# Performance work log

Measured on AMD Instinct MI355X. Metric: run time of the kernel, lower is better.

The kernel has to match this reference:

```python
import jax, jax.numpy as jnp
import numpy as np

DISTANCE_W = 1.0
ANGLE_W = 1.0
EPS = 1e-12  # matches F.normalize eps


def setup_inputs() -> dict:
    key = jax.random.key(0)
    k1, k2 = jax.random.split(key)
    student_emb = jax.random.normal(k1, (1024, 512), dtype=jnp.float32)
    teacher_emb = jax.random.normal(k2, (1024, 512), dtype=jnp.float32)
    return {"student_emb": student_emb, "teacher_emb": teacher_emb}


def _pairwise_similarity(emb):
    # F.normalize(emb, dim=1) then emb @ emb.T -> [N, N] cosine similarity
    norm = jnp.maximum(jnp.linalg.norm(emb, axis=1, keepdims=True), EPS)
    en = emb / norm
    return en @ en.T


def _angle_similarity(emb):
    # ||e_i - e_j||^2 for all pairs, computed via the GEMM expansion
    # (same math as the N x N x D broadcast in the original, no O(N^2 D) tensor)
    sq = jnp.sum(emb * emb, axis=1)  # [N]
    gram = emb @ emb.T               # [N, N]
    return sq[:, None] + sq[None, :] - 2.0 * gram


def reference(student_emb, teacher_emb):
    loss_dist = jnp.mean((_pairwise_similarity(student_emb) - _pairwise_similarity(teacher_emb)) ** 2)
    loss_angle = jnp.mean((_angle_similarity(student_emb) - _angle_similarity(teacher_emb)) ** 2)
    return DISTANCE_W * loss_dist + ANGLE_W * loss_angle
```

## Files before the change

kernel.cpp:

```cpp
#include <hip/hip_runtime.h>

typedef short short8 __attribute__((ext_vector_type(8)));
typedef float f32x16 __attribute__((ext_vector_type(16)));
typedef unsigned short ushort;
typedef unsigned long long u64;

#define DD 512
#define NBLK 272
#define MAGIC 0x9E3779B97F4A7C15ULL


__device__ __forceinline__ short to_bf16(float f) {
    unsigned int u = __float_as_uint(f);
    u += 0x7FFFu + ((u >> 16) & 1u);
    return (short)(u >> 16);
}

__device__ __forceinline__ short8 pack8(float4 a, float4 b) {
    short8 r;
    r[0] = to_bf16(a.x); r[1] = to_bf16(a.y); r[2] = to_bf16(a.z); r[3] = to_bf16(a.w);
    r[4] = to_bf16(b.x); r[5] = to_bf16(b.y); r[6] = to_bf16(b.z); r[7] = to_bf16(b.w);
    return r;
}

__device__ __forceinline__ float dot4(float4 v) {
    return v.x*v.x + v.y*v.y + v.z*v.z + v.w*v.w;
}

__global__ __launch_bounds__(128) void rkd_one(const float* __restrict__ S,
                                               const float* __restrict__ T,
                                               u64* __restrict__ done_tag,
                                               float* __restrict__ done_val,
                                               float* __restrict__ out) {
    __shared__ ushort tiles[2][12288];
    __shared__ float statI[4][32];
    __shared__ float statJ[4][64];
    __shared__ float wsum[2];

    const int t   = threadIdx.x;
    const int blk = blockIdx.x;

    int rem = blk, a = 0;
    for (;;) { int cnt = 16 - (a >> 1); if (rem < cnt) break; rem -= cnt; ++a; }
    const int b2 = (a >> 1) + rem;
    const int I = a * 32;
    const int J = b2 * 64;

    const int w = t >> 6;
    const int L = t & 63;
    const int c = L & 31;
    const int h = L >> 5;
    const int colsel = w * 32;
    const int lrow   = L >> 3;
    const int c8     = (L & 7) ^ lrow;

    const float* gsrc[12];
    int ldst[12];
    #pragma unroll
    for (int j = 0; j < 12; ++j) {
        const int q = w * 12 + j;
        const float* gm; int gbase, lo, sub;
        if (q < 4)       { gm = S; gbase = I; sub = q;      lo = 0;    }
        else if (q < 8)  { gm = T; gbase = I; sub = q - 4;  lo = 2048; }
        else if (q < 16) { gm = S; gbase = J; sub = q - 8;  lo = 4096; }
        else             { gm = T; gbase = J; sub = q - 16; lo = 8192; }
        gsrc[j] = gm + (size_t)(gbase + sub * 8 + lrow) * DD + c8 * 8;
        ldst[j] = lo + sub * 512 + L * 8;
    }

    float4 rv[12][2];
    float  sqp[12];
    #pragma unroll
    for (int j = 0; j < 12; ++j) sqp[j] = 0.0f;

    f32x16 accS, accT;
    #pragma unroll
    for (int i2 = 0; i2 < 16; ++i2) { accS[i2] = 0.0f; accT[i2] = 0.0f; }

    #pragma unroll
    for (int j = 0; j < 12; ++j) {
        rv[j][0] = ((const float4*)gsrc[j])[0];
        rv[j][1] = ((const float4*)gsrc[j])[1];
    }

    for (int i = 0; i < 8; ++i) {
        __syncthreads();
        ushort* db = &tiles[i & 1][0];
        #pragma unroll
        for (int j = 0; j < 12; ++j) {
            sqp[j] += dot4(rv[j][0]) + dot4(rv[j][1]);
            *(short8*)(db + ldst[j]) = pack8(rv[j][0], rv[j][1]);
        }
        __syncthreads();
        if (i < 7) {
            #pragma unroll
            for (int j = 0; j < 12; ++j) {
                rv[j][0] = ((const float4*)(gsrc[j] + (i + 1) * 64))[0];
                rv[j][1] = ((const float4*)(gsrc[j] + (i + 1) * 64))[1];
            }
        }
        const ushort* base = &tiles[i & 1][0];
        #pragma unroll
        for (int step = 0; step < 4; ++step) {
            const int us = ((step * 2 + h) ^ (c & 7)) * 8;
            short8 afS = *(const short8*)(base + c * 64 + us);
            short8 afT = *(const short8*)(base + 2048 + c * 64 + us);
            short8 bS8 = *(const short8*)(base + 4096 + (colsel + c) * 64 + us);
            short8 bT8 = *(const short8*)(base + 8192 + (colsel + c) * 64 + us);
            accS = __builtin_amdgcn_mfma_f32_32x32x16_bf16(afS, bS8, accS, 0, 0, 0);
            accT = __builtin_amdgcn_mfma_f32_32x32x16_bf16(afT, bT8, accT, 0, 0, 0);
        }
    }

    #pragma unroll
    for (int j = 0; j < 12; ++j) {
        float s = sqp[j];
        s += __shfl_xor(s, 1);
        s += __shfl_xor(s, 2);
        s += __shfl_xor(s, 4);
        if ((L & 7) == 0) {
            const float rn = 1.0f / fmaxf(sqrtf(s), 1e-12f);
            const int q = w * 12 + j;
            if (q < 4)       { statI[0][q*8        + lrow] = s; statI[2][q*8        + lrow] = rn; }
            else if (q < 8)  { statI[1][(q-4)*8    + lrow] = s; statI[3][(q-4)*8    + lrow] = rn; }
            else if (q < 16) { statJ[0][(q-8)*8    + lrow] = s; statJ[2][(q-8)*8    + lrow] = rn; }
            else             { statJ[1][(q-16)*8   + lrow] = s; statJ[3][(q-16)*8   + lrow] = rn; }
        }
    }
    __syncthreads();

    const int colg = colsel + c;
    const int jg   = J + colg;
    const float js  = statJ[0][colg], jt  = statJ[1][colg];
    const float rjs = statJ[2][colg], rjt = statJ[3][colg];

    float local = 0.0f;
    #pragma unroll
    for (int reg = 0; reg < 16; ++reg) {
        const int rowg = (reg & 3) + 8 * (reg >> 2) + 4 * h;
        const int ig = I + rowg;
        float wgt = (jg > ig) ? 2.0f : ((jg == ig) ? 1.0f : 0.0f);
        float is  = statI[0][rowg], it  = statI[1][rowg];
        float ris = statI[2][rowg], rit = statI[3][rowg];
        float gs = accS[reg], gt = accT[reg];
        float d1 = gs * ris * rjs - gt * rit * rjt;
        float d2 = (is + js - 2.0f * gs) - (it + jt - 2.0f * gt);
        local += wgt * (d1 * d1 + d2 * d2);
    }

    #pragma unroll
    for (int off = 32; off > 0; off >>= 1) local += __shfl_down(local, off);
    if (L == 0) wsum[w] = local;
    __syncthreads();

    if (t == 0) {
        done_val[blk] = wsum[0] + wsum[1];
        __threadfence();
        __hip_atomic_store(&done_tag[blk], MAGIC,
                           __ATOMIC_RELAXED, __HIP_MEMORY_SCOPE_AGENT);
    }

    if (blk == NBLK - 1) {
        for (int i2 = t; i2 < NBLK; i2 += 128)
            while (__hip_atomic_load(&done_tag[i2], __ATOMIC_RELAXED,
                                     __HIP_MEMORY_SCOPE_AGENT) != MAGIC)
                __builtin_amdgcn_s_sleep(2);
        __syncthreads();
        __threadfence();
        float part = 0.0f;
        for (int i2 = t; i2 < NBLK; i2 += 128) part += done_val[i2];
        #pragma unroll
        for (int off = 32; off > 0; off >>= 1) part += __shfl_down(part, off);
        if ((t & 63) == 0) wsum[t >> 6] = part;
        __syncthreads();
        if (t == 0) out[0] = (wsum[0] + wsum[1]) * (1.0f / 1048576.0f);
    }
}

extern "C" void kernel_launch(void* const* d_in, const int* in_sizes, int n_in,
                              void* d_out, int out_size, void* d_ws, size_t ws_size,
                              hipStream_t stream) {
    const float* S = (const float*)d_in[0];
    const float* T = (const float*)d_in[1];
    char* ws = (char*)d_ws;
    u64*   done_tag = (u64*)ws;
    float* done_val = (float*)(ws + 4096);

    rkd_one<<<NBLK, 128, 0, stream>>>(S, T, done_tag, done_val, (float*)d_out);
}
```

Before: 83.38 us.

## Stage fp32 tiles via direct global-to-LDS loads and convert at MFMA time

Replaces the register-staged load, convert and LDS store pipeline with async global_load_lds that copies fp32 data straight into shared memory with double buffering. Conversion to bf16 moves to the MFMA operand read and uses the packed v_cvt_pk_bf16_f32 instruction. Row squared norms are now accumulated from the LDS-read fragments. This drops VGPR pressure and one barrier per iteration, at the cost of twice the LDS traffic for fp32 tiles, twice the k-iterations, and redundant conversions across waves.

```diff
diff --git a/kernel.cpp b/kernel.cpp
--- a/kernel.cpp
+++ b/kernel.cpp
@@ -3,6 +3,7 @@
 typedef short short8 __attribute__((ext_vector_type(8)));
 typedef float f32x16 __attribute__((ext_vector_type(16)));
 typedef unsigned short ushort;
+typedef unsigned int u32;
 typedef unsigned long long u64;
 
 #define DD 512
@@ -10,17 +11,19 @@
 #define MAGIC 0x9E3779B97F4A7C15ULL
 
 
-__device__ __forceinline__ short to_bf16(float f) {
-    unsigned int u = __float_as_uint(f);
-    u += 0x7FFFu + ((u >> 16) & 1u);
-    return (short)(u >> 16);
+__device__ __forceinline__ u32 cvt_pk_bf16(float lo, float hi) {
+    u32 r;
+    asm("v_cvt_pk_bf16_f32 %0, %1, %2" : "=v"(r) : "v"(lo), "v"(hi));
+    return r;
 }
 
-__device__ __forceinline__ short8 pack8(float4 a, float4 b) {
-    short8 r;
-    r[0] = to_bf16(a.x); r[1] = to_bf16(a.y); r[2] = to_bf16(a.z); r[3] = to_bf16(a.w);
-    r[4] = to_bf16(b.x); r[5] = to_bf16(b.y); r[6] = to_bf16(b.z); r[7] = to_bf16(b.w);
-    return r;
+__device__ __forceinline__ short8 pack_bf8(float4 a, float4 b) {
+    union { u32 u[4]; short8 s; } r;
+    r.u[0] = cvt_pk_bf16(a.x, a.y);
+    r.u[1] = cvt_pk_bf16(a.z, a.w);
+    r.u[2] = cvt_pk_bf16(b.x, b.y);
+    r.u[3] = cvt_pk_bf16(b.z, b.w);
+    return r.s;
 }
 
 __device__ __forceinline__ float dot4(float4 v) {
@@ -32,7 +35,7 @@
                                                u64* __restrict__ done_tag,
                                                float* __restrict__ done_val,
                                                float* __restrict__ out) {
-    __shared__ ushort tiles[2][12288];
+    __shared__ float tiles[2][6144];
     __shared__ float statI[4][32];
     __shared__ float statJ[4][64];
     __shared__ float wsum[2];
@@ -61,70 +64,73 @@
         const int q = w * 12 + j;
         const float* gm; int gbase, lo, sub;
         if (q < 4)       { gm = S; gbase = I; sub = q;      lo = 0;    }
-        else if (q < 8)  { gm = T; gbase = I; sub = q - 4;  lo = 2048; }
-        else if (q < 16) { gm = S; gbase = J; sub = q - 8;  lo = 4096; }
-        else             { gm = T; gbase = J; sub = q - 16; lo = 8192; }
-        gsrc[j] = gm + (size_t)(gbase + sub * 8 + lrow) * DD + c8 * 8;
-        ldst[j] = lo + sub * 512 + L * 8;
+        else if (q < 8)  { gm = T; gbase = I; sub = q - 4;  lo = 1024; }
+        else if (q < 16) { gm = S; gbase = J; sub = q - 8;  lo = 2048; }
+        else             { gm = T; gbase = J; sub = q - 16; lo = 4096; }
+        gsrc[j] = gm + (size_t)(gbase + sub * 8 + lrow) * DD + c8 * 4;
+        ldst[j] = lo + sub * 256 + L * 4;
     }
-
-    float4 rv[12][2];
-    float  sqp[12];
-    #pragma unroll
-    for (int j = 0; j < 12; ++j) sqp[j] = 0.0f;
 
     f32x16 accS, accT;
     #pragma unroll
     for (int i2 = 0; i2 < 16; ++i2) { accS[i2] = 0.0f; accT[i2] = 0.0f; }
+    float sqp[4] = {0.0f, 0.0f, 0.0f, 0.0f};
 
     #pragma unroll
-    for (int j = 0; j < 12; ++j) {
-        rv[j][0] = ((const float4*)gsrc[j])[0];
-        rv[j][1] = ((const float4*)gsrc[j])[1];
-    }
+    for (int j = 0; j < 12; ++j)
+        __builtin_amdgcn_global_load_lds(
+            (const __attribute__((address_space(1))) void*)(gsrc[j]),
+            (__attribute__((address_space(3))) void*)(&tiles[0][0] + ldst[j]), 16, 0, 0);
 
-    for (int i = 0; i < 8; ++i) {
+    for (int i = 0; i < 16; ++i) {
         __syncthreads();
-        ushort* db = &tiles[i & 1][0];
+        if (i < 15) {
+            const int k0 = (i + 1) * 32;
+            float* nb = &tiles[(i + 1) & 1][0];
+            #pragma unroll
+            for (int j = 0; j < 12; ++j)
+                __builtin_amdgcn_global_load_lds(
+                    (const __attribute__((address_space(1))) void*)(gsrc[j] + k0),
+                    (__attribute__((address_space(3))) void*)(nb + ldst[j]), 16, 0, 0);
+        }
+        const float* base = &tiles[i & 1][0];
+        const float* Ar = base + c * 32;
+        const float* Br = base + (colsel + c) * 32;
         #pragma unroll
-        for (int j = 0; j < 12; ++j) {
-            sqp[j] += dot4(rv[j][0]) + dot4(rv[j][1]);
-            *(short8*)(db + ldst[j]) = pack8(rv[j][0], rv[j][1]);
-        }
-        __syncthreads();
-        if (i < 7) {
-            #pragma unroll
-            for (int j = 0; j < 12; ++j) {
-                rv[j][0] = ((const float4*)(gsrc[j] + (i + 1) * 64))[0];
-                rv[j][1] = ((const float4*)(gsrc[j] + (i + 1) * 64))[1];
-            }
-        }
-        const ushort* base = &tiles[i & 1][0];
-        #pragma unroll
-        for (int step = 0; step < 4; ++step) {
-            const int us = ((step * 2 + h) ^ (c & 7)) * 8;
-            short8 afS = *(const short8*)(base + c * 64 + us);
-            short8 afT = *(const short8*)(base + 2048 + c * 64 + us);
-            short8 bS8 = *(const short8*)(base + 4096 + (colsel + c) * 64 + us);
-            short8 bT8 = *(const short8*)(base + 8192 + (colsel + c) * 64 + us);
-            accS = __builtin_amdgcn_mfma_f32_32x32x16_bf16(afS, bS8, accS, 0, 0, 0);
-            accT = __builtin_amdgcn_mfma_f32_32x32x16_bf16(afT, bT8, accT, 0, 0, 0);
+        for (int s = 0; s < 2; ++s) {
+            const int oc0 = (((s * 4) + h * 2)     ^ (c & 7)) * 4;
+            const int oc1 = (((s * 4) + h * 2 + 1) ^ (c & 7)) * 4;
+            float4 a0 = *(const float4*)(Ar + oc0);
+            float4 a1 = *(const float4*)(Ar + oc1);
+            float4 t0 = *(const float4*)(Ar + 1024 + oc0);
+            float4 t1 = *(const float4*)(Ar + 1024 + oc1);
+            float4 b0 = *(const float4*)(Br + 2048 + oc0);
+            float4 b1 = *(const float4*)(Br + 2048 + oc1);
+            float4 u0 = *(const float4*)(Br + 4096 + oc0);
+            float4 u1 = *(const float4*)(Br + 4096 + oc1);
+            sqp[0] += dot4(a0) + dot4(a1);
+            sqp[1] += dot4(t0) + dot4(t1);
+            sqp[2] += dot4(b0) + dot4(b1);
+            sqp[3] += dot4(u0) + dot4(u1);
+            accS = __builtin_amdgcn_mfma_f32_32x32x16_bf16(pack_bf8(a0, a1),
+                                                           pack_bf8(b0, b1), accS, 0, 0, 0);
+            accT = __builtin_amdgcn_mfma_f32_32x32x16_bf16(pack_bf8(t0, t1),
+                                                           pack_bf8(u0, u1), accT, 0, 0, 0);
         }
     }
 
-    #pragma unroll
-    for (int j = 0; j < 12; ++j) {
-        float s = sqp[j];
-        s += __shfl_xor(s, 1);
-        s += __shfl_xor(s, 2);
-        s += __shfl_xor(s, 4);
-        if ((L & 7) == 0) {
-            const float rn = 1.0f / fmaxf(sqrtf(s), 1e-12f);
-            const int q = w * 12 + j;
-            if (q < 4)       { statI[0][q*8        + lrow] = s; statI[2][q*8        + lrow] = rn; }
-            else if (q < 8)  { statI[1][(q-4)*8    + lrow] = s; statI[3][(q-4)*8    + lrow] = rn; }
-            else if (q < 16) { statJ[0][(q-8)*8    + lrow] = s; statJ[2][(q-8)*8    + lrow] = rn; }
-            else             { statJ[1][(q-16)*8   + lrow] = s; statJ[3][(q-16)*8   + lrow] = rn; }
+    {
+        const float sAS = sqp[0] + __shfl_xor(sqp[0], 32);
+        const float sAT = sqp[1] + __shfl_xor(sqp[1], 32);
+        const float sBS = sqp[2] + __shfl_xor(sqp[2], 32);
+        const float sBT = sqp[3] + __shfl_xor(sqp[3], 32);
+        if (h == 0) {
+            if (w == 0) {
+                statI[0][c] = sAS; statI[2][c] = 1.0f / fmaxf(sqrtf(sAS), 1e-12f);
+                statI[1][c] = sAT; statI[3][c] = 1.0f / fmaxf(sqrtf(sAT), 1e-12f);
+            }
+            statJ[0][colsel + c] = sBS; statJ[2][colsel + c] = 1.0f / fmaxf(sqrtf(sBS), 1e-12f);
+            statJ[1][colsel + c] = sBT; statJ[3][colsel + c] = 1.0f / fmaxf(sqrtf(sBT), 1e-12f);
         }
     }
     __syncthreads();
```

Result: faster. 79.98 us (-4.1%).
